# Performance work log

Hardware: AMD Instinct MI355X
Metric: run time of the kernel (lower is better)

## Reference

```python
import jax, jax.numpy as jnp
import numpy as np

B, T, VOCAB, EMB, H = 2048, 80, 80, 8, 256
FORGET_BIAS = 1.0  # tf BasicLSTMCell default


def setup_inputs() -> dict:
    key = jax.random.key(0)
    ks = jax.random.split(key, 8)
    s_in1 = 1.0 / np.sqrt(EMB + H)
    s_in2 = 1.0 / np.sqrt(H + H)
    return {
        "features": jax.random.randint(ks[0], (B, T), 0, VOCAB, dtype=jnp.int32),
        "labels": jax.random.randint(ks[1], (B,), 0, VOCAB, dtype=jnp.int32),
        "embedding": jax.random.normal(ks[2], (VOCAB, EMB), jnp.float32) * 0.1,
        "W1": jax.random.normal(ks[3], (EMB + H, 4 * H), jnp.float32) * s_in1,
        "b1": jnp.zeros((4 * H,), jnp.float32),
        "W2": jax.random.normal(ks[4], (H + H, 4 * H), jnp.float32) * s_in2,
        "b2": jnp.zeros((4 * H,), jnp.float32),
        "Wd": jax.random.normal(ks[5], (H, VOCAB), jnp.float32) * (1.0 / np.sqrt(H)),
        "bd": jnp.zeros((VOCAB,), jnp.float32),
    }


def _lstm_layer(x, W, b):
    # x: [B, T, D] -> outputs h: [B, T, H]; BasicLSTMCell gate order (i, j, f, o)
    bsz = x.shape[0]
    c0 = jnp.zeros((bsz, H), x.dtype)
    h0 = jnp.zeros((bsz, H), x.dtype)

    def step(carry, xt):
        c, h = carry
        gates = jnp.concatenate([xt, h], axis=-1) @ W + b  # [B, 4H]
        i, j, f, o = jnp.split(gates, 4, axis=-1)
        c_new = c * jax.nn.sigmoid(f + FORGET_BIAS) + jax.nn.sigmoid(i) * jnp.tanh(j)
        h_new = jnp.tanh(c_new) * jax.nn.sigmoid(o)
        return (c_new, h_new), h_new

    _, hs = jax.lax.scan(step, (c0, h0), jnp.swapaxes(x, 0, 1))  # hs: [T, B, H]
    return jnp.swapaxes(hs, 0, 1)


def reference(features, labels, embedding, W1, b1, W2, b2, Wd, bd):
    x = embedding[features]                     # [B, T, EMB]
    h1 = _lstm_layer(x, W1, b1)                 # [B, T, H]
    h2 = _lstm_layer(h1, W2, b2)                # [B, T, H]
    logits = h2[:, -1, :] @ Wd + bd             # [B, VOCAB]
    onehot = jax.nn.one_hot(labels, VOCAB, dtype=logits.dtype)
    loss = -jnp.mean(jnp.sum(onehot * jax.nn.log_softmax(logits, axis=-1), axis=-1))
    return loss
```

## Files before the change

### kernel.cpp

```cpp
#include <hip/hip_runtime.h>
#include <cstdint>

#define B_SZ   2048
#define T_SZ   80
#define VOCABN 80
#define EMBN   8
#define HID    256
#define G4     1024
#define NTHR   512
#define HP     272

typedef __bf16 bf16;
typedef __attribute__((ext_vector_type(4))) int    i32x4;
typedef __attribute__((ext_vector_type(4))) float  f32x4;
typedef __attribute__((ext_vector_type(4))) unsigned short u16x4;

__device__ __forceinline__ float sigf(float x)   { return 1.0f / (1.0f + __expf(-x)); }
__device__ __forceinline__ float tanhf2(float x) { return 1.0f - 2.0f / (__expf(2.0f * x) + 1.0f); }

__device__ __forceinline__ unsigned short f2bf(float f) {
    union { float f; unsigned int u; } v; v.f = f;
    unsigned int u = v.u;
    return (unsigned short)((u + 0x7FFFu + ((u >> 16) & 1u)) >> 16);
}
__device__ __forceinline__ float bf2f(unsigned short h) {
    union { unsigned int u; float f; } v; v.u = ((unsigned int)h) << 16;
    return v.f;
}
__device__ __forceinline__ signed char q8(float h) {
    int q = (int)rintf(h * 127.0f);
    q = q > 127 ? 127 : (q < -127 ? -127 : q);
    return (signed char)q;
}

#define WP8_OFF  0ull
#define EG2_OFF  786432ull
#define SW_OFF   1114112ull
#define C1G_OFF  1126400ull
#define C2G_OFF  3223552ull
#define H2P_OFF  5320704ull
#define H1C_OFF  5844992ull
#define FIXED_WS 5844992ull
#define PER_TC   4718592ull

__global__ void prep_scale(const float* __restrict__ W1, const float* __restrict__ W2,
                           float* __restrict__ sw) {
    int idx = blockIdx.x * blockDim.x + threadIdx.x;
    if (idx >= 3 * 1024) return;
    int s = idx >> 10, c = idx & 1023;
    float m = 0.0f;
    for (int r = 0; r < 256; ++r) {
        float v = (s == 0) ? W1[(EMBN + r) * G4 + c]
                : (s == 1) ? W2[r * G4 + c]
                           : W2[(256 + r) * G4 + c];
        m = fmaxf(m, fabsf(v));
    }
    sw[idx] = m * (1.0f / 127.0f) + 1e-20f;
}

__global__ void prep_pack(const float* __restrict__ W1, const float* __restrict__ W2,
                          const float* __restrict__ sw, signed char* __restrict__ wp8) {
    int idx = blockIdx.x * blockDim.x + threadIdx.x;
    if (idx >= 3 * 4 * 64 * 64) return;
    int lane = idx & 63, nt = (idx >> 6) & 63, ks = (idx >> 12) & 3, s = idx >> 14;
    int lc = lane & 15, lg = lane >> 4;
    int scol = (nt & 3) * 256 + (nt >> 3) * 32 + ((nt >> 2) & 1) * 16 + lc;
    float sc = 1.0f / sw[s * 1024 + scol];
#pragma unroll
    for (int e = 0; e < 16; ++e) {
        int row = ks * 64 + lg * 16 + e;
        float v = (s == 0) ? W1[(EMBN + row) * G4 + scol]
                : (s == 1) ? W2[row * G4 + scol]
                           : W2[(256 + row) * G4 + scol];
        int q = (int)rintf(v * sc);
        q = q > 127 ? 127 : (q < -127 ? -127 : q);
        wp8[(size_t)idx * 16 + e] = (signed char)q;
    }
}

__global__ void prep_eg2(const float* __restrict__ emb, const float* __restrict__ W1,
                         const float* __restrict__ b1, float* __restrict__ eg2) {
    int idx = blockIdx.x * blockDim.x + threadIdx.x;
    if (idx >= VOCABN * 256) return;
    int v = idx >> 8, h = idx & 255;
#pragma unroll
    for (int g = 0; g < 4; ++g) {
        int c = g * 256 + h;
        float s = b1[c];
#pragma unroll
        for (int e = 0; e < EMBN; ++e) s += emb[v * EMBN + e] * W1[e * G4 + c];
        eg2[(size_t)idx * 4 + g] = s;
    }
}

__global__ __launch_bounds__(NTHR, 2)
void lstm_l1(const int* __restrict__ feat,
             const signed char* __restrict__ wp8A, const float* __restrict__ swA,
             const float* __restrict__ eg2,
             signed char* __restrict__ h1c, float* __restrict__ c1g,
             int t0, int TC)
{
    __shared__ __align__(16) signed char wlds[2][64][1024];
    __shared__ __align__(16) signed char h1s[2][16 * HP];
    __shared__ unsigned char toks8[8 * T_SZ];

    const int tid  = threadIdx.x;
    const int lane = tid & 63;
    const int wid  = tid >> 6;
    const int lc   = lane & 15;
    const int lg   = lane >> 4;
    const int hfl  = lg >> 1;
    const int lgl  = lg & 1;
    const int bblk = blockIdx.x;
    const int b0   = bblk * 8;
    const int t1   = t0 + TC;

    for (int i = tid; i < 2 * 16 * HP; i += NTHR) h1s[0][i] = 0;
    for (int i = tid; i < 8 * T_SZ; i += NTHR) {
        int r = i / T_SZ, t = i - r * T_SZ;
        toks8[i] = (unsigned char)feat[(b0 + r) * T_SZ + t];
    }
    for (int i = tid; i < 2 * 64 * 64; i += NTHR)
        *(i32x4*)&wlds[0][0][(size_t)i * 16] =
            *(const i32x4*)&wp8A[(size_t)(2 * 64 * 64 + i) * 16];

    const int hcolp = wid * 32 + hfl * 16 + lc;
    float c1[4] = {0.f, 0.f, 0.f, 0.f};
    if (t0 > 0) {
        __syncthreads();
        for (int i = tid; i < 8 * 256; i += NTHR) {
            int row = i >> 8, col = i & 255;
            h1s[0][row * HP + col] = h1c[((size_t)(b0 + row) * TC + (TC - 1)) * 256 + col];
        }
#pragma unroll
        for (int r = 0; r < 4; ++r)
            c1[r] = c1g[(size_t)(b0 + lgl * 4 + r) * 256 + hcolp];
    }
    __syncthreads();

    i32x4 wreg[16];
#pragma unroll
    for (int ks = 0; ks < 2; ++ks)
#pragma unroll
        for (int j = 0; j < 8; ++j)
            wreg[ks * 8 + j] = *(const i32x4*)&wp8A[(size_t)((ks * 64 + wid * 8 + j) * 64 + lane) * 16];

    float ssv[4];
#pragma unroll
    for (int g = 0; g < 4; ++g)
        ssv[g] = swA[g * 256 + hcolp] * (1.0f / 127.0f);

    const i32x4 zi = {0, 0, 0, 0};

    for (int t = t0; t < t1; ++t) {
        const int rb_ = t & 1;
        const signed char* hr = h1s[rb_];
        signed char* hw = h1s[rb_ ^ 1];

        i32x4 ia0[4], ia1[4];
#pragma unroll
        for (int g = 0; g < 4; ++g) { ia0[g] = zi; ia1[g] = zi; }
#pragma unroll
        for (int ks = 0; ks < 4; ++ks) {
            i32x4 afr = *(const i32x4*)&hr[lc * HP + ks * 64 + lg * 16];
#pragma unroll
            for (int g = 0; g < 4; ++g) {
                i32x4 w0 = (ks < 2) ? wreg[ks * 8 + g]
                         : *(const i32x4*)&wlds[ks - 2][wid * 8 + g][(size_t)lane * 16];
                ia0[g] = __builtin_amdgcn_mfma_i32_16x16x64_i8(afr, w0, ia0[g], 0, 0, 0);
                i32x4 w1 = (ks < 2) ? wreg[ks * 8 + 4 + g]
                         : *(const i32x4*)&wlds[ks - 2][wid * 8 + 4 + g][(size_t)lane * 16];
                ia1[g] = __builtin_amdgcn_mfma_i32_16x16x64_i8(afr, w1, ia1[g], 0, 0, 0);
            }
        }
#pragma unroll
        for (int r = 0; r < 4; ++r) {
            const int row = lgl * 4 + r;
            const int tok = toks8[row * T_SZ + t];
            f32x4 e4 = *(const f32x4*)&eg2[((size_t)tok * 256 + hcolp) * 4];
            float gv[4];
#pragma unroll
            for (int g = 0; g < 4; ++g) {
                int v1  = __shfl(ia1[g][r], lane & 31);
                int sel = hfl ? v1 : ia0[g][r];
                gv[g] = ssv[g] * (float)sel + e4[g];
            }
            float cn = c1[r] * sigf(gv[2] + 1.0f) + sigf(gv[0]) * tanhf2(gv[1]);
            float h  = tanhf2(cn) * sigf(gv[3]);
            c1[r] = cn;
            signed char qv = q8(h);
            hw[row * HP + hcolp] = qv;
            h1c[((size_t)(b0 + row) * TC + (t - t0)) * 256 + hcolp] = qv;
        }
        __syncthreads();
    }
    if (t1 < T_SZ) {
#pragma unroll
        for (int r = 0; r < 4; ++r)
            c1g[(size_t)(b0 + lgl * 4 + r) * 256 + hcolp] = c1[r];
    }
}

__global__ __launch_bounds__(NTHR, 2)
void gx_gemm(const signed char* __restrict__ h1c,
             const signed char* __restrict__ wp8G, const float* __restrict__ swG,
             const float* __restrict__ b2, unsigned short* __restrict__ gxc, int TC)
{
    __shared__ __align__(16) signed char wlds[2][64][1024];
    __shared__ __align__(16) signed char hbuf[16 * HP];

    const int tid  = threadIdx.x;
    const int lane = tid & 63;
    const int wid  = tid >> 6;
    const int lc   = lane & 15;
    const int lg   = lane >> 4;
    const int bblk = blockIdx.x;

    for (int i = tid; i < 2 * 64 * 64; i += NTHR)
        *(i32x4*)&wlds[0][0][(size_t)i * 16] =
            *(const i32x4*)&wp8G[(size_t)(2 * 64 * 64 + i) * 16];

    i32x4 wreg[16];
#pragma unroll
    for (int ks = 0; ks < 2; ++ks)
#pragma unroll
        for (int j = 0; j < 8; ++j)
            wreg[ks * 8 + j] = *(const i32x4*)&wp8G[(size_t)((ks * 64 + wid * 8 + j) * 64 + lane) * 16];

    float ssg[8], b2v[8];
#pragma unroll
    for (int j = 0; j < 8; ++j) {
        int scol = (j & 3) * 256 + wid * 32 + ((j >> 2) & 1) * 16 + lc;
        ssg[j] = swG[scol] * (1.0f / 127.0f);
        b2v[j] = b2[scol];
    }

    const i32x4 zi = {0, 0, 0, 0};
    const int m    = tid >> 5;
    const int col0 = (tid & 31) * 8;
    const int np   = TC >> 1;

    unsigned long long sreg =
        *(const unsigned long long*)&h1c[((size_t)(bblk * 8 + (m >> 1)) * TC + (m & 1)) * 256 + col0];

    for (int tt = 0; tt < np; ++tt) {
        __syncthreads();
        *(unsigned long long*)&hbuf[m * HP + col0] = sreg;
        __syncthreads();
        if (tt + 1 < np)
            sreg = *(const unsigned long long*)
                &h1c[((size_t)(bblk * 8 + (m >> 1)) * TC + (tt + 1) * 2 + (m & 1)) * 256 + col0];

        i32x4 acc[8];
#pragma unroll
        for (int j = 0; j < 8; ++j) acc[j] = zi;
#pragma unroll
        for (int ks = 0; ks < 4; ++ks) {
            i32x4 afr = *(const i32x4*)&hbuf[lc * HP + ks * 64 + lg * 16];
#pragma unroll
            for (int j = 0; j < 8; ++j) {
                i32x4 w = (ks < 2) ? wreg[ks * 8 + j]
                        : *(const i32x4*)&wlds[ks - 2][wid * 8 + j][(size_t)lane * 16];
                acc[j] = __builtin_amdgcn_mfma_i32_16x16x64_i8(afr, w, acc[j], 0, 0, 0);
            }
        }
#pragma unroll
        for (int j = 0; j < 8; ++j) {
            const int nt = wid * 8 + j;
#pragma unroll
            for (int r = 0; r < 4; ++r) {
                size_t addr = ((((size_t)bblk * TC + tt * 2 + (r & 1)) * 64 + nt) * 16 + lc) * 8
                              + 2 * lg + (r >> 1);
                gxc[addr] = f2bf(ssg[j] * (float)acc[j][r] + b2v[j]);
            }
        }
    }
}

__global__ __launch_bounds__(NTHR, 2)
void lstm_l2(const signed char* __restrict__ wp8B, const float* __restrict__ swB,
             const unsigned short* __restrict__ gxc,
             const int* __restrict__ labels,
             const float* __restrict__ Wd, const float* __restrict__ bd,
             float* __restrict__ out, float* __restrict__ c2g,
             signed char* __restrict__ h2p, int t0, int TC)
{
    __shared__ __align__(16) signed char wlds[2][64][1024];
    __shared__ __align__(16) signed char h2s[2][16 * HP];
    __shared__ float logitb[8][VOCABN + 1];
    __shared__ float lossb[8];

    const int tid  = threadIdx.x;
    const int lane = tid & 63;
    const int wid  = tid >> 6;
    const int lc   = lane & 15;
    const int lg   = lane >> 4;
    const int hfl  = lg >> 1;
    const int lgl  = lg & 1;
    const int bblk = blockIdx.x;
    const int b0   = bblk * 8;
    const int t1   = t0 + TC;

    for (int i = tid; i < 2 * 16 * HP; i += NTHR) h2s[0][i] = 0;
    for (int i = tid; i < 2 * 64 * 64; i += NTHR)
        *(i32x4*)&wlds[0][0][(size_t)i * 16] =
            *(const i32x4*)&wp8B[(size_t)(2 * 64 * 64 + i) * 16];

    const int hcolp = wid * 32 + hfl * 16 + lc;
    float c2[4] = {0.f, 0.f, 0.f, 0.f};
    if (t0 > 0) {
        __syncthreads();
        for (int i = tid; i < 8 * 256; i += NTHR) {
            int row = i >> 8, col = i & 255;
            h2s[0][row * HP + col] = h2p[(size_t)(b0 + row) * 256 + col];
        }
#pragma unroll
        for (int r = 0; r < 4; ++r)
            c2[r] = c2g[(size_t)(b0 + lgl * 4 + r) * 256 + hcolp];
    }
    __syncthreads();

    i32x4 wreg[16];
#pragma unroll
    for (int ks = 0; ks < 2; ++ks)
#pragma unroll
        for (int j = 0; j < 8; ++j)
            wreg[ks * 8 + j] = *(const i32x4*)&wp8B[(size_t)((ks * 64 + wid * 8 + j) * 64 + lane) * 16];

    float ssv[4];
#pragma unroll
    for (int g = 0; g < 4; ++g)
        ssv[g] = swB[g * 256 + hcolp] * (1.0f / 127.0f);

    const i32x4 zi = {0, 0, 0, 0};

    for (int t = t0; t < t1; ++t) {
        const int rb_ = t & 1;
        const signed char* hr = h2s[rb_];
        signed char* hw = h2s[rb_ ^ 1];

        u16x4 gxv[4];
#pragma unroll
        for (int g = 0; g < 4; ++g) {
            const int nt = wid * 8 + hfl * 4 + g;
            size_t addr = ((((size_t)bblk * TC + (t - t0)) * 64 + nt) * 16 + lc) * 8 + 4 * lgl;
            gxv[g] = *(const u16x4*)(gxc + addr);
        }

        i32x4 ia0[4], ia1[4];
#pragma unroll
        for (int g = 0; g < 4; ++g) { ia0[g] = zi; ia1[g] = zi; }
#pragma unroll
        for (int ks = 0; ks < 4; ++ks) {
            i32x4 afr = *(const i32x4*)&hr[lc * HP + ks * 64 + lg * 16];
#pragma unroll
            for (int g = 0; g < 4; ++g) {
                i32x4 w0 = (ks < 2) ? wreg[ks * 8 + g]
                         : *(const i32x4*)&wlds[ks - 2][wid * 8 + g][(size_t)lane * 16];
                ia0[g] = __builtin_amdgcn_mfma_i32_16x16x64_i8(afr, w0, ia0[g], 0, 0, 0);
                i32x4 w1 = (ks < 2) ? wreg[ks * 8 + 4 + g]
                         : *(const i32x4*)&wlds[ks - 2][wid * 8 + 4 + g][(size_t)lane * 16];
                ia1[g] = __builtin_amdgcn_mfma_i32_16x16x64_i8(afr, w1, ia1[g], 0, 0, 0);
            }
        }
#pragma unroll
        for (int r = 0; r < 4; ++r) {
            const int row = lgl * 4 + r;
            float gv[4];
#pragma unroll
            for (int g = 0; g < 4; ++g) {
                int v1  = __shfl(ia1[g][r], lane & 31);
                int sel = hfl ? v1 : ia0[g][r];
                gv[g] = ssv[g] * (float)sel + bf2f(gxv[g][r]);
            }
            float cn = c2[r] * sigf(gv[2] + 1.0f) + sigf(gv[0]) * tanhf2(gv[1]);
            float h  = tanhf2(cn) * sigf(gv[3]);
            c2[r] = cn;
            hw[row * HP + hcolp] = q8(h);
        }
        __syncthreads();
    }

    if (t1 < T_SZ) {
#pragma unroll
        for (int r = 0; r < 4; ++r)
            c2g[(size_t)(b0 + lgl * 4 + r) * 256 + hcolp] = c2[r];
        for (int i = tid; i < 8 * 256; i += NTHR) {
            int row = i >> 8, col = i & 255;
            h2p[(size_t)(b0 + row) * 256 + col] = h2s[0][row * HP + col];
        }
        return;
    }

    const signed char* h2fin = h2s[0];
    for (int pp = tid; pp < 8 * VOCABN; pp += NTHR) {
        int row = pp / VOCABN, v = pp - row * VOCABN;
        float s = bd[v];
        for (int k = 0; k < HID; ++k)
            s += ((float)h2fin[row * HP + k] * (1.0f / 127.0f)) * Wd[k * VOCABN + v];
        logitb[row][v] = s;
    }
    __syncthreads();
    if (tid < 8) {
        float mx = -1e30f;
        for (int v = 0; v < VOCABN; ++v) mx = fmaxf(mx, logitb[tid][v]);
        float s = 0.f;
        for (int v = 0; v < VOCABN; ++v) s += __expf(logitb[tid][v] - mx);
        int lab = labels[b0 + tid];
        lossb[tid] = mx + __logf(s) - logitb[tid][lab];
    }
    __syncthreads();
    if (tid == 0) {
        float s = 0.f;
#pragma unroll
        for (int r = 0; r < 8; ++r) s += lossb[r];
        atomicAdd(out, s * (1.0f / (float)B_SZ));
    }
}

extern "C" void kernel_launch(void* const* d_in, const int* in_sizes, int n_in,
                              void* d_out, int out_size, void* d_ws, size_t ws_size,
                              hipStream_t stream)
{
    (void)in_sizes; (void)n_in; (void)out_size;
    const int*   feat   = (const int*)d_in[0];
    const int*   labels = (const int*)d_in[1];
    const float* emb    = (const float*)d_in[2];
    const float* W1     = (const float*)d_in[3];
    const float* b1     = (const float*)d_in[4];
    const float* W2     = (const float*)d_in[5];
    const float* b2     = (const float*)d_in[6];
    const float* Wd     = (const float*)d_in[7];
    const float* bd     = (const float*)d_in[8];
    float* out = (float*)d_out;
    char* ws = (char*)d_ws;

    (void)hipMemsetAsync(d_out, 0, sizeof(float), stream);

    int TC = 2;
    {
        const int tcs[8] = {80, 40, 20, 16, 10, 8, 4, 2};
        for (int i = 0; i < 8; ++i)
            if (FIXED_WS + (size_t)tcs[i] * PER_TC <= ws_size) { TC = tcs[i]; break; }
    }

    signed char* wp8  = (signed char*)(ws + WP8_OFF);
    float*       eg2  = (float*)(ws + EG2_OFF);
    float*       sw   = (float*)(ws + SW_OFF);
    float*       c1g  = (float*)(ws + C1G_OFF);
    float*       c2g  = (float*)(ws + C2G_OFF);
    signed char* h2p  = (signed char*)(ws + H2P_OFF);
    signed char* h1c  = (signed char*)(ws + H1C_OFF);
    unsigned short* gxc = (unsigned short*)(ws + H1C_OFF + (size_t)TC * 524288ull);

    const signed char* wp8A = wp8;
    const signed char* wp8G = wp8 + 262144;
    const signed char* wp8B = wp8 + 524288;
    const float* swA = sw;
    const float* swG = sw + 1024;
    const float* swB = sw + 2048;

    prep_scale<<<(3 * 1024 + 255) / 256, 256, 0, stream>>>(W1, W2, sw);
    prep_pack<<<(3 * 4 * 64 * 64 + 255) / 256, 256, 0, stream>>>(W1, W2, sw, wp8);
    prep_eg2<<<(VOCABN * 256 + 255) / 256, 256, 0, stream>>>(emb, W1, b1, eg2);

    for (int t0 = 0; t0 < T_SZ; t0 += TC) {
        lstm_l1<<<256, NTHR, 0, stream>>>(feat, wp8A, swA, eg2, h1c, c1g, t0, TC);
        gx_gemm<<<256, NTHR, 0, stream>>>(h1c, wp8G, swG, b2, gxc, TC);
        lstm_l2<<<256, NTHR, 0, stream>>>(wp8B, swB, gxc, labels, Wd, bd,
                                          out, c2g, h2p, t0, TC);
    }
}
```

Measured before the change: 529.9 us.

## Split LSTM gate epilogue rows across doubled thread blocks in both recurrent kernels

Both recurrent LSTM kernels now launch 1024 threads per block. The upper 512 threads recompute the same int8 MFMA gate products but apply the nonlinear cell update to only two of each lane's four batch rows, so the per-step serial epilogue per thread is halved. Global addressing for the h1 output and gx input is strength-reduced into incrementing pointers, and the gx loads shrink to two elements. The cost is duplicated MFMA and LDS reads per step and tighter register limits from the new launch bounds, which risks spills given the register-resident weights.

```diff
diff --git a/kernel.cpp b/kernel.cpp
--- a/kernel.cpp
+++ b/kernel.cpp
@@ -8,12 +8,14 @@
 #define HID    256
 #define G4     1024
 #define NTHR   512
+#define NTHRR  1024
 #define HP     272
 
 typedef __bf16 bf16;
 typedef __attribute__((ext_vector_type(4))) int    i32x4;
 typedef __attribute__((ext_vector_type(4))) float  f32x4;
 typedef __attribute__((ext_vector_type(4))) unsigned short u16x4;
+typedef __attribute__((ext_vector_type(2))) unsigned short u16x2;
 
 __device__ __forceinline__ float sigf(float x)   { return 1.0f / (1.0f + __expf(-x)); }
 __device__ __forceinline__ float tanhf2(float x) { return 1.0f - 2.0f / (__expf(2.0f * x) + 1.0f); }
@@ -93,7 +95,26 @@
     }
 }
 
-__global__ __launch_bounds__(NTHR, 2)
+#define PW1(rj, rr_) do {                                                       \
+    const int row_ = lgl * 4 + (rj);                                            \
+    const int tok_ = toks8[row_ * T_SZ + t];                                    \
+    f32x4 e4_ = *(const f32x4*)&eg2[((size_t)tok_ * 256 + hcolp) * 4];          \
+    float gv_[4];                                                               \
+    _Pragma("unroll")                                                           \
+    for (int g_ = 0; g_ < 4; ++g_) {                                            \
+        int v1_  = __shfl(ia1[g_][rj], lane & 31);                              \
+        int sel_ = hfl ? v1_ : ia0[g_][rj];                                     \
+        gv_[g_] = ssv[g_] * (float)sel_ + e4_[g_];                              \
+    }                                                                           \
+    float cn_ = c1[rr_] * sigf(gv_[2] + 1.0f) + sigf(gv_[0]) * tanhf2(gv_[1]);  \
+    float h_  = tanhf2(cn_) * sigf(gv_[3]);                                     \
+    c1[rr_] = cn_;                                                              \
+    signed char qv_ = q8(h_);                                                   \
+    hw[row_ * HP + hcolp] = qv_;                                                \
+    *((rr_) ? pB : pA) = qv_;                                                   \
+} while (0)
+
+__global__ __launch_bounds__(NTHRR, 4)
 void lstm_l1(const int* __restrict__ feat,
              const signed char* __restrict__ wp8A, const float* __restrict__ swA,
              const float* __restrict__ eg2,
@@ -106,7 +127,8 @@
 
     const int tid  = threadIdx.x;
     const int lane = tid & 63;
-    const int wid  = tid >> 6;
+    const int wid  = (tid >> 6) & 7;
+    const int rsel = tid >> 9;
     const int lc   = lane & 15;
     const int lg   = lane >> 4;
     const int hfl  = lg >> 1;
@@ -115,26 +137,27 @@
     const int b0   = bblk * 8;
     const int t1   = t0 + TC;
 
-    for (int i = tid; i < 2 * 16 * HP; i += NTHR) h1s[0][i] = 0;
-    for (int i = tid; i < 8 * T_SZ; i += NTHR) {
+    for (int i = tid; i < 2 * 16 * HP; i += NTHRR) h1s[0][i] = 0;
+    for (int i = tid; i < 8 * T_SZ; i += NTHRR) {
         int r = i / T_SZ, t = i - r * T_SZ;
         toks8[i] = (unsigned char)feat[(b0 + r) * T_SZ + t];
     }
-    for (int i = tid; i < 2 * 64 * 64; i += NTHR)
+    for (int i = tid; i < 2 * 64 * 64; i += NTHRR)
         *(i32x4*)&wlds[0][0][(size_t)i * 16] =
             *(const i32x4*)&wp8A[(size_t)(2 * 64 * 64 + i) * 16];
 
     const int hcolp = wid * 32 + hfl * 16 + lc;
-    float c1[4] = {0.f, 0.f, 0.f, 0.f};
+    const int rowA  = lgl * 4 + rsel * 2;
+    float c1[2] = {0.f, 0.f};
     if (t0 > 0) {
         __syncthreads();
-        for (int i = tid; i < 8 * 256; i += NTHR) {
+        for (int i = tid; i < 8 * 256; i += NTHRR) {
             int row = i >> 8, col = i & 255;
             h1s[0][row * HP + col] = h1c[((size_t)(b0 + row) * TC + (TC - 1)) * 256 + col];
         }
 #pragma unroll
-        for (int r = 0; r < 4; ++r)
-            c1[r] = c1g[(size_t)(b0 + lgl * 4 + r) * 256 + hcolp];
+        for (int rr = 0; rr < 2; ++rr)
+            c1[rr] = c1g[(size_t)(b0 + rowA + rr) * 256 + hcolp];
     }
     __syncthreads();
 
@@ -149,6 +172,9 @@
 #pragma unroll
     for (int g = 0; g < 4; ++g)
         ssv[g] = swA[g * 256 + hcolp] * (1.0f / 127.0f);
+
+    signed char* pA = h1c + ((size_t)(b0 + rowA) * TC) * 256 + hcolp;
+    signed char* pB = pA + (size_t)TC * 256;
 
     const i32x4 zi = {0, 0, 0, 0};
 
@@ -173,31 +199,15 @@
                 ia1[g] = __builtin_amdgcn_mfma_i32_16x16x64_i8(afr, w1, ia1[g], 0, 0, 0);
             }
         }
-#pragma unroll
-        for (int r = 0; r < 4; ++r) {
-            const int row = lgl * 4 + r;
-            const int tok = toks8[row * T_SZ + t];
-            f32x4 e4 = *(const f32x4*)&eg2[((size_t)tok * 256 + hcolp) * 4];
-            float gv[4];
-#pragma unroll
-            for (int g = 0; g < 4; ++g) {
-                int v1  = __shfl(ia1[g][r], lane & 31);
-                int sel = hfl ? v1 : ia0[g][r];
-                gv[g] = ssv[g] * (float)sel + e4[g];
-            }
-            float cn = c1[r] * sigf(gv[2] + 1.0f) + sigf(gv[0]) * tanhf2(gv[1]);
-            float h  = tanhf2(cn) * sigf(gv[3]);
-            c1[r] = cn;
-            signed char qv = q8(h);
-            hw[row * HP + hcolp] = qv;
-            h1c[((size_t)(b0 + row) * TC + (t - t0)) * 256 + hcolp] = qv;
-        }
+        if (rsel == 0) { PW1(0, 0); PW1(1, 1); }
+        else           { PW1(2, 0); PW1(3, 1); }
+        pA += 256; pB += 256;
         __syncthreads();
     }
     if (t1 < T_SZ) {
 #pragma unroll
-        for (int r = 0; r < 4; ++r)
-            c1g[(size_t)(b0 + lgl * 4 + r) * 256 + hcolp] = c1[r];
+        for (int rr = 0; rr < 2; ++rr)
+            c1g[(size_t)(b0 + rowA + rr) * 256 + hcolp] = c1[rr];
     }
 }
 
@@ -277,7 +287,22 @@
     }
 }
 
-__global__ __launch_bounds__(NTHR, 2)
+#define PW2(rj, rr_) do {                                                       \
+    const int row_ = lgl * 4 + (rj);                                            \
+    float gv_[4];                                                               \
+    _Pragma("unroll")                                                           \
+    for (int g_ = 0; g_ < 4; ++g_) {                                            \
+        int v1_  = __shfl(ia1[g_][rj], lane & 31);                              \
+        int sel_ = hfl ? v1_ : ia0[g_][rj];                                     \
+        gv_[g_] = ssv[g_] * (float)sel_ + bf2f(gx2[g_][rr_]);                   \
+    }                                                                           \
+    float cn_ = c2[rr_] * sigf(gv_[2] + 1.0f) + sigf(gv_[0]) * tanhf2(gv_[1]);  \
+    float h_  = tanhf2(cn_) * sigf(gv_[3]);                                     \
+    c2[rr_] = cn_;                                                              \
+    hw[row_ * HP + hcolp] = q8(h_);                                             \
+} while (0)
+
+__global__ __launch_bounds__(NTHRR, 4)
 void lstm_l2(const signed char* __restrict__ wp8B, const float* __restrict__ swB,
              const unsigned short* __restrict__ gxc,
              const int* __restrict__ labels,
@@ -292,7 +317,8 @@
 
     const int tid  = threadIdx.x;
     const int lane = tid & 63;
-    const int wid  = tid >> 6;
+    const int wid  = (tid >> 6) & 7;
+    const int rsel = tid >> 9;
     const int lc   = lane & 15;
     const int lg   = lane >> 4;
     const int hfl  = lg >> 1;
@@ -301,22 +327,23 @@
     const int b0   = bblk * 8;
     const int t1   = t0 + TC;
 
-    for (int i = tid; i < 2 * 16 * HP; i += NTHR) h2s[0][i] = 0;
-    for (int i = tid; i < 2 * 64 * 64; i += NTHR)
+    for (int i = tid; i < 2 * 16 * HP; i += NTHRR) h2s[0][i] = 0;
+    for (int i = tid; i < 2 * 64 * 64; i += NTHRR)
         *(i32x4*)&wlds[0][0][(size_t)i * 16] =
             *(const i32x4*)&wp8B[(size_t)(2 * 64 * 64 + i) * 16];
 
     const int hcolp = wid * 32 + hfl * 16 + lc;
-    float c2[4] = {0.f, 0.f, 0.f, 0.f};
+    const int rowA  = lgl * 4 + rsel * 2;
+    float c2[2] = {0.f, 0.f};
     if (t0 > 0) {
         __syncthreads();
-        for (int i = tid; i < 8 * 256; i += NTHR) {
+        for (int i = tid; i < 8 * 256; i += NTHRR) {
             int row = i >> 8, col = i & 255;
             h2s[0][row * HP + col] = h2p[(size_t)(b0 + row) * 256 + col];
         }
 #pragma unroll
-        for (int r = 0; r < 4; ++r)
-            c2[r] = c2g[(size_t)(b0 + lgl * 4 + r) * 256 + hcolp];
+        for (int rr = 0; rr < 2; ++rr)
+            c2[rr] = c2g[(size_t)(b0 + rowA + rr) * 256 + hcolp];
     }
     __syncthreads();
 
@@ -331,6 +358,13 @@
 #pragma unroll
     for (int g = 0; g < 4; ++g)
         ssv[g] = swB[g * 256 + hcolp] * (1.0f / 127.0f);
+
+    const unsigned short* pg[4];
+#pragma unroll
+    for (int g = 0; g < 4; ++g) {
+        const int nt = wid * 8 + hfl * 4 + g;
+        pg[g] = gxc + (((size_t)bblk * TC * 64 + nt) * 16 + lc) * 8 + 4 * lgl + rsel * 2;
+    }
 
     const i32x4 zi = {0, 0, 0, 0};
 
@@ -339,12 +373,11 @@
         const signed char* hr = h2s[rb_];
         signed char* hw = h2s[rb_ ^ 1];
 
-        u16x4 gxv[4];
+        u16x2 gx2[4];
 #pragma unroll
         for (int g = 0; g < 4; ++g) {
-            const int nt = wid * 8 + hfl * 4 + g;
-            size_t addr = ((((size_t)bblk * TC + (t - t0)) * 64 + nt) * 16 + lc) * 8 + 4 * lgl;
-            gxv[g] = *(const u16x4*)(gxc + addr);
+            gx2[g] = *(const u16x2*)pg[g];
+            pg[g] += 8192;
         }
 
         i32x4 ia0[4], ia1[4];
@@ -363,29 +396,16 @@
                 ia1[g] = __builtin_amdgcn_mfma_i32_16x16x64_i8(afr, w1, ia1[g], 0, 0, 0);
             }
         }
-#pragma unroll
-        for (int r = 0; r < 4; ++r) {
-            const int row = lgl * 4 + r;
-            float gv[4];
-#pragma unroll
-            for (int g = 0; g < 4; ++g) {
-                int v1  = __shfl(ia1[g][r], lane & 31);
-                int sel = hfl ? v1 : ia0[g][r];
-                gv[g] = ssv[g] * (float)sel + bf2f(gxv[g][r]);
-            }
-            float cn = c2[r] * sigf(gv[2] + 1.0f) + sigf(gv[0]) * tanhf2(gv[1]);
-            float h  = tanhf2(cn) * sigf(gv[3]);
-            c2[r] = cn;
-            hw[row * HP + hcolp] = q8(h);
-        }
+        if (rsel == 0) { PW2(0, 0); PW2(1, 1); }
+        else           { PW2(2, 0); PW2(3, 1); }
         __syncthreads();
     }
 
     if (t1 < T_SZ) {
 #pragma unroll
-        for (int r = 0; r < 4; ++r)
-            c2g[(size_t)(b0 + lgl * 4 + r) * 256 + hcolp] = c2[r];
-        for (int i = tid; i < 8 * 256; i += NTHR) {
+        for (int rr = 0; rr < 2; ++rr)
+            c2g[(size_t)(b0 + rowA + rr) * 256 + hcolp] = c2[rr];
+        for (int i = tid; i < 8 * 256; i += NTHRR) {
             int row = i >> 8, col = i & 255;
             h2p[(size_t)(b0 + row) * 256 + col] = h2s[0][row * HP + col];
         }
@@ -393,7 +413,7 @@
     }
 
     const signed char* h2fin = h2s[0];
-    for (int pp = tid; pp < 8 * VOCABN; pp += NTHR) {
+    for (int pp = tid; pp < 8 * VOCABN; pp += NTHRR) {
         int row = pp / VOCABN, v = pp - row * VOCABN;
         float s = bd[v];
         for (int k = 0; k < HID; ++k)
@@ -465,9 +485,9 @@
     prep_eg2<<<(VOCABN * 256 + 255) / 256, 256, 0, stream>>>(emb, W1, b1, eg2);
 
     for (int t0 = 0; t0 < T_SZ; t0 += TC) {
-        lstm_l1<<<256, NTHR, 0, stream>>>(feat, wp8A, swA, eg2, h1c, c1g, t0, TC);
+        lstm_l1<<<256, NTHRR, 0, stream>>>(feat, wp8A, swA, eg2, h1c, c1g, t0, TC);
         gx_gemm<<<256, NTHR, 0, stream>>>(h1c, wp8G, swG, b2, gxc, TC);
-        lstm_l2<<<256, NTHR, 0, stream>>>(wp8B, swB, gxc, labels, Wd, bd,
-                                          out, c2g, h2p, t0, TC);
-    }
-}
+        lstm_l2<<<256, NTHRR, 0, stream>>>(wp8B, swB, gxc, labels, Wd, bd,
+                                           out, c2g, h2p, t0, TC);
+    }
+}
```

New measurement: 1.025 ms. +93.4%, slower.
